# Optimization experiments

Measured on AMD Instinct MI355X. Metric: run time of the kernel, lower is better.

## Reference

```python
import jax, jax.numpy as jnp
import numpy as np

N_KNN = 20
BN_EPS = 1e-5
LRELU_SLOPE = 0.2


def setup_inputs() -> dict:
    key = jax.random.key(0)
    k1, k2, k3 = jax.random.split(key, 3)
    B, C, N = 4, 3, 8192
    x = jax.random.normal(k1, (B, C, N), dtype=jnp.float32)
    # Conv2d(1, 16, 1): weight [16,1,1,1] -> flatten to [16]; bias [16]
    conv_w = jax.random.normal(k2, (16,), dtype=jnp.float32) * (1.0 / np.sqrt(1.0))
    conv_b = jax.random.normal(k3, (16,), dtype=jnp.float32) * 0.01
    gamma = jnp.ones((16,), dtype=jnp.float32)
    beta = jnp.zeros((16,), dtype=jnp.float32)
    return {"x": x, "conv_w": conv_w, "conv_b": conv_b, "gamma": gamma, "beta": beta}


def reference(x, conv_w, conv_b, gamma, beta):
    # x: [B, C, N]
    pts = jnp.transpose(x, (0, 2, 1))  # [B, N, C]
    sq = jnp.sum(pts * pts, axis=-1)  # [B, N]
    # pairwise squared distances, clamped for numerical safety
    d2 = sq[:, :, None] + sq[:, None, :] - 2.0 * jnp.einsum("bnc,bmc->bnm", pts, pts)
    d2 = jnp.maximum(d2, 0.0)
    # safe sqrt: zero gradient at zero distance (matches torch.cdist behavior)
    dist = jnp.where(d2 > 0, jnp.sqrt(jnp.where(d2 > 0, d2, 1.0)), 0.0)  # [B, N, N]
    # k smallest distances = k largest of negated
    neg_topk, _ = jax.lax.top_k(-dist, N_KNN)
    knn = -neg_topk  # [B, N, K], ascending
    # 1x1 conv (1 -> 16 channels): feat[b,c,n,k] = w[c]*knn[b,n,k] + b[c]
    feat = knn[:, None, :, :] * conv_w[None, :, None, None] + conv_b[None, :, None, None]  # [B,16,N,K]
    # BatchNorm2d in training mode: per-channel stats over (B, N, K), biased variance
    mean = jnp.mean(feat, axis=(0, 2, 3), keepdims=True)
    var = jnp.mean((feat - mean) ** 2, axis=(0, 2, 3), keepdims=True)
    xhat = (feat - mean) * jax.lax.rsqrt(var + BN_EPS)
    y = gamma[None, :, None, None] * xhat + beta[None, :, None, None]
    # LeakyReLU(0.2)
    y = jnp.where(y >= 0, y, LRELU_SLOPE * y)
    # max over k neighbors
    return jnp.max(y, axis=-1)  # [B, 16, N]
```

## Files before the change

kernel.cpp:

```cpp
#include <hip/hip_runtime.h>
#include <stdint.h>

#define NPTS  8192
#define NB    4
#define KNN   20
#define NROWS (NB * NPTS)
#define NGROUPS (NROWS / 64)
#define MTOTF 655360.0f
#define WPB   8
#define BLK   (WPB * 64)
#define SLICE (NPTS / WPB)
#define HALF  (NPTS / 2)
#define SLICE2 (HALF / WPB)
#define LSTR  (KNN + 1)
#define CAP   12
#define CAP2  16
#define NGRID (2 * NGROUPS)
#define NEG_INF -3.0e38f

__device__ __forceinline__ float med3f(float a, float b, float c) {
    return __builtin_amdgcn_fmed3f(a, b, c);
}

__device__ __forceinline__ unsigned enc_f(float f) {
    unsigned u = __float_as_uint(f);
    return (u & 0x80000000u) ? ~u : (u | 0x80000000u);
}
__device__ __forceinline__ float dec_f(unsigned u) {
    return __uint_as_float((u & 0x80000000u) ? (u & 0x7fffffffu) : ~u);
}

__device__ __forceinline__ void insert_t(float arr[KNN], float t) {
#pragma unroll
    for (int j = KNN - 1; j > 0; --j) arr[j] = med3f(t, arr[j - 1], arr[j]);
    arr[0] = fmaxf(arr[0], t);
}

__device__ __forceinline__ void flush_buf(float arr[KNN], int& cnt,
    const float* bufw, int lane, unsigned* threshS) {
#pragma unroll
    for (int s = 0; s < CAP; ++s) {
        const float v = bufw[s * 64 + lane];
        insert_t(arr, (s < cnt) ? v : NEG_INF);
    }
    cnt = 0;
    atomicMax(&threshS[lane], enc_f(arr[KNN - 1]));
}

__device__ __forceinline__ void flush_dyn(float arr[KNN], int& cnt,
    const float* bufw, int lane, unsigned* threshS) {
#pragma unroll
    for (int s0 = 0; s0 < CAP2; s0 += 4) {
        if (__any(cnt > s0)) {
#pragma unroll
            for (int s = s0; s < s0 + 4; ++s) {
                const float v = bufw[s * 64 + lane];
                insert_t(arr, (s < cnt) ? v : NEG_INF);
            }
        }
    }
    cnt = 0;
    atomicMax(&threshS[lane], enc_f(arr[KNN - 1]));
}

__device__ __forceinline__ void finalize_row(
    float arr[KNN], float px, float py, float pz, int row, int lane,
    float* __restrict__ kmaxA, float* __restrict__ kminA, float* __restrict__ acc)
{
    const float pn2 = px * px + py * py + pz * pz;
    float sum = 0.f, sum2 = 0.f, dmin = 0.f, dmax = 0.f;
#pragma unroll
    for (int k = 0; k < KNN; ++k) {
        float d2 = fmaxf(fmaf(-2.f, arr[k], pn2), 0.f);
        float d = sqrtf(d2);
        sum += d; sum2 += d2;
        if (k == 0) dmin = d;
        dmax = d;
    }
    kmaxA[row] = dmax;
    kminA[row] = dmin;
#pragma unroll
    for (int o = 32; o; o >>= 1) {
        sum  += __shfl_down(sum,  o, 64);
        sum2 += __shfl_down(sum2, o, 64);
    }
    if (lane == 0) { atomicAdd(acc, sum); atomicAdd(acc + 1, sum2); }
}

__global__ __launch_bounds__(256) void prep_kernel(
    const float* __restrict__ x, float4* __restrict__ tile4,
    float* __restrict__ acc, int* __restrict__ ticket)
{
    const int i = blockIdx.x * 256 + threadIdx.x;
    const int b = i >> 13;
    const int m = i & (NPTS - 1);
    const float* xb = x + b * 3 * NPTS;
    const float qx = xb[m], qy = xb[NPTS + m], qz = xb[2 * NPTS + m];
    tile4[i] = make_float4(qx, qy, qz, -0.5f * (qx * qx + qy * qy + qz * qz));
    if (i < 2) acc[i] = 0.f;
    if (ticket && i < NGROUPS) ticket[i] = 0;
}

__global__ __launch_bounds__(BLK, 8) void knn_fused_kernel(
    const float* __restrict__ x, const float4* __restrict__ tile4,
    float* __restrict__ part, int* __restrict__ ticket,
    float* __restrict__ kmaxA, float* __restrict__ kminA, float* __restrict__ acc)
{
    __shared__ float shmem[WPB * CAP2 * 64];
    __shared__ unsigned threshS[64];

    const int tid  = threadIdx.x;
    const int lane = tid & 63;
    const int wave = __builtin_amdgcn_readfirstlane(tid >> 6);
    const int rb   = blockIdx.x >> 1;
    const int half = blockIdx.x & 1;
    const int rowBase = rb * 64;
    const int row  = rowBase + lane;
    const int b    = rowBase >> 13;
    const int n    = row & (NPTS - 1);
    const float* xb = x + b * 3 * NPTS;
    const float px = xb[n];
    const float py = xb[NPTS + n];
    const float pz = xb[2 * NPTS + n];

    if (tid < 64) threshS[tid] = enc_f(NEG_INF);

    float arr[KNN];
#pragma unroll
    for (int j = 0; j < KNN; ++j) arr[j] = NEG_INF;
    float* bufw = shmem + wave * (CAP2 * 64);
    __syncthreads();

    const float4* __restrict__ tp = tile4 + b * NPTS + half * HALF + wave * SLICE2;

#pragma unroll 8
    for (int i = 0; i < 32; ++i) {
        const float4 q = tp[i];
        insert_t(arr, fmaf(q.x, px, fmaf(q.y, py, fmaf(q.z, pz, q.w))));
    }
    atomicMax(&threshS[lane], enc_f(arr[KNN - 1]));

    int cnt = 0;
    for (int c = 1; c < SLICE2 / 32; ++c) {
        float th = dec_f(*(volatile unsigned*)(threshS + lane));
        const float4* tq = tp + c * 32;
        for (int g = 0; g < 8; ++g) {
#pragma unroll
            for (int u = 0; u < 4; ++u) {
                const float4 q = tq[g * 4 + u];
                const float t = fmaf(q.x, px, fmaf(q.y, py, fmaf(q.z, pz, q.w)));
                bufw[cnt * 64 + lane] = t;
                cnt += (t > th);
            }
            if (__any(cnt > CAP2 - 4)) {
                flush_dyn(arr, cnt, bufw, lane, threshS);
                th = dec_f(*(volatile unsigned*)(threshS + lane));
            }
        }
    }
    if (__any(cnt > 0)) flush_dyn(arr, cnt, bufw, lane, threshS);
    __syncthreads();

    float* ml = shmem;
    if (wave & 1) {
        float* d = ml + (wave >> 1) * (64 * LSTR) + lane * LSTR;
#pragma unroll
        for (int k = 0; k < KNN; ++k) d[k] = arr[k];
    }
    __syncthreads();
    if (!(wave & 1)) {
        const float* s = ml + (wave >> 1) * (64 * LSTR) + lane * LSTR;
#pragma unroll
        for (int k = 0; k < KNN; ++k) insert_t(arr, s[k]);
    }
    __syncthreads();
    if (!(wave & 1) && (wave & 2)) {
        float* d = ml + (wave >> 2) * (64 * LSTR) + lane * LSTR;
#pragma unroll
        for (int k = 0; k < KNN; ++k) d[k] = arr[k];
    }
    __syncthreads();
    if ((wave & 3) == 0) {
        const float* s = ml + (wave >> 2) * (64 * LSTR) + lane * LSTR;
#pragma unroll
        for (int k = 0; k < KNN; ++k) insert_t(arr, s[k]);
    }
    __syncthreads();
    if (wave == 4) {
        float* d = ml + lane * LSTR;
#pragma unroll
        for (int k = 0; k < KNN; ++k) d[k] = arr[k];
    }
    __syncthreads();
    if (wave == 0) {
        const float* s = ml + lane * LSTR;
#pragma unroll
        for (int k = 0; k < KNN; ++k) insert_t(arr, s[k]);

        float* dst = part + (row * 2 + half) * KNN;
#pragma unroll
        for (int k = 0; k < KNN; ++k)
            __hip_atomic_store(&dst[k], arr[k], __ATOMIC_RELAXED,
                               __HIP_MEMORY_SCOPE_AGENT);
        asm volatile("s_waitcnt vmcnt(0)" ::: "memory");

        int old = 0;
        if (lane == 0)
            old = __hip_atomic_fetch_add(&ticket[rb], 1, __ATOMIC_RELAXED,
                                         __HIP_MEMORY_SCOPE_AGENT);
        old = __shfl(old, 0, 64);
        if (old == 1) {
            const float* srcp = part + (row * 2 + (half ^ 1)) * KNN;
#pragma unroll
            for (int k = 0; k < KNN; ++k) {
                const float v = __hip_atomic_load(&srcp[k], __ATOMIC_RELAXED,
                                                  __HIP_MEMORY_SCOPE_AGENT);
                insert_t(arr, v);
            }
            finalize_row(arr, px, py, pz, row, lane, kmaxA, kminA, acc);
        }
    }
}

__global__ __launch_bounds__(256) void out_elem_kernel(
    const float* __restrict__ kmaxA, const float* __restrict__ kminA,
    const float* __restrict__ acc,
    const float* __restrict__ w, const float* __restrict__ gamma,
    const float* __restrict__ beta, float* __restrict__ out)
{
    const int T = blockIdx.x * 256 + threadIdx.x;
    const int n  = T & (NPTS - 1);
    const int bc = T >> 13;
    const int c  = bc & 15;
    const int b  = bc >> 4;
    const float mu  = acc[0] * (1.0f / MTOTF);
    float var = acc[1] * (1.0f / MTOTF) - mu * mu;
    var = fmaxf(var, 0.f);
    const float wc = w[c];
    const float a  = gamma[c] * wc * rsqrtf(wc * wc * var + 1e-5f);
    const float d  = beta[c] - a * mu;
    const float km = (a >= 0.f) ? kmaxA[b * NPTS + n] : kminA[b * NPTS + n];
    float v = a * km + d;
    v = (v >= 0.f) ? v : 0.2f * v;
    out[T] = v;
}


__global__ __launch_bounds__(BLK, 8) void knn_kernel(
    const float* __restrict__ x, const float4* __restrict__ tile4,
    float* __restrict__ kmaxA, float* __restrict__ kminA, float* __restrict__ acc)
{
    __shared__ float shmem[(WPB - 1) * 64 * LSTR];
    __shared__ unsigned threshS[64];

    const int tid  = threadIdx.x;
    const int lane = tid & 63;
    const int wave = __builtin_amdgcn_readfirstlane(tid >> 6);
    const int rowBase = blockIdx.x * 64;
    const int row  = rowBase + lane;
    const int b    = rowBase >> 13;
    const int n    = row & (NPTS - 1);
    const float* xb = x + b * 3 * NPTS;
    const float px = xb[n];
    const float py = xb[NPTS + n];
    const float pz = xb[2 * NPTS + n];

    if (tid < 64) threshS[tid] = enc_f(NEG_INF);

    float arr[KNN];
#pragma unroll
    for (int j = 0; j < KNN; ++j) arr[j] = NEG_INF;
    float* bufw = shmem + wave * (CAP * 64);
    int cnt = 0;
    __syncthreads();

    const float4* __restrict__ tp = tile4 + b * NPTS + wave * SLICE;
    float th = NEG_INF;
    for (int c = 0; c < SLICE / 32; ++c) {
        th = dec_f(*(volatile unsigned*)(threshS + lane));
        const float4* tq = tp + c * 32;
        for (int g = 0; g < 8; ++g) {
#pragma unroll
            for (int u = 0; u < 4; ++u) {
                const float4 q = tq[g * 4 + u];
                const float t = fmaf(q.x, px, fmaf(q.y, py, fmaf(q.z, pz, q.w)));
                if (t > th) { bufw[cnt * 64 + lane] = t; ++cnt; }
            }
            if (__any(cnt > CAP - 4)) {
                flush_buf(arr, cnt, bufw, lane, threshS);
                th = dec_f(*(volatile unsigned*)(threshS + lane));
            }
        }
    }
    if (__any(cnt > 0)) flush_buf(arr, cnt, bufw, lane, threshS);
    __syncthreads();

    if (wave > 0) {
        float* dst = shmem + ((wave - 1) * 64 + lane) * LSTR;
#pragma unroll
        for (int j = 0; j < KNN; ++j) dst[j] = arr[j];
    }
    __syncthreads();

    if (wave == 0) {
        for (int wsrc = 0; wsrc < WPB - 1; ++wsrc) {
            const float* src = shmem + (wsrc * 64 + lane) * LSTR;
#pragma unroll
            for (int k = 0; k < KNN; ++k) insert_t(arr, src[k]);
        }
        finalize_row(arr, px, py, pz, row, lane, kmaxA, kminA, acc);
    }
}

__global__ __launch_bounds__(BLK) void knn_kernel_lds(
    const float* __restrict__ x,
    float* __restrict__ kmaxA, float* __restrict__ kminA, float* __restrict__ acc)
{
    __shared__ float4 tile[2048];
    __shared__ float  lists[(WPB - 1) * 64 * LSTR];

    const int tid  = threadIdx.x;
    const int lane = tid & 63;
    const int wave = tid >> 6;
    const int rowBase = blockIdx.x * 64;
    const int row  = rowBase + lane;
    const int b    = rowBase >> 13;
    const int n    = row & (NPTS - 1);
    const float* xb = x + b * 3 * NPTS;
    const float px = xb[n];
    const float py = xb[NPTS + n];
    const float pz = xb[2 * NPTS + n];

    float arr[KNN];
#pragma unroll
    for (int j = 0; j < KNN; ++j) arr[j] = NEG_INF;

    for (int t0 = 0; t0 < NPTS; t0 += 2048) {
        __syncthreads();
        const int i4 = tid * 4;
        const float4 qx4 = *(const float4*)(xb + t0 + i4);
        const float4 qy4 = *(const float4*)(xb + NPTS + t0 + i4);
        const float4 qz4 = *(const float4*)(xb + 2 * NPTS + t0 + i4);
        tile[i4 + 0] = make_float4(qx4.x, qy4.x, qz4.x, -0.5f * (qx4.x*qx4.x + qy4.x*qy4.x + qz4.x*qz4.x));
        tile[i4 + 1] = make_float4(qx4.y, qy4.y, qz4.y, -0.5f * (qx4.y*qx4.y + qy4.y*qy4.y + qz4.y*qz4.y));
        tile[i4 + 2] = make_float4(qx4.z, qy4.z, qz4.z, -0.5f * (qx4.z*qx4.z + qy4.z*qy4.z + qz4.z*qz4.z));
        tile[i4 + 3] = make_float4(qx4.w, qy4.w, qz4.w, -0.5f * (qx4.w*qx4.w + qy4.w*qy4.w + qz4.w*qz4.w));
        __syncthreads();
        const float4* basep = tile + wave * 256;
#pragma unroll 4
        for (int i = 0; i < 256; ++i) {
            const float4 q = basep[i];
            float t = fmaf(q.x, px, fmaf(q.y, py, fmaf(q.z, pz, q.w)));
            insert_t(arr, t);
        }
    }
    __syncthreads();

    if (wave > 0) {
        float* dst = lists + ((wave - 1) * 64 + lane) * LSTR;
#pragma unroll
        for (int j = 0; j < KNN; ++j) dst[j] = arr[j];
    }
    __syncthreads();

    if (wave == 0) {
        for (int wsrc = 0; wsrc < WPB - 1; ++wsrc) {
            const float* src = lists + (wsrc * 64 + lane) * LSTR;
#pragma unroll
            for (int k = 0; k < KNN; ++k) insert_t(arr, src[k]);
        }
        finalize_row(arr, px, py, pz, row, lane, kmaxA, kminA, acc);
    }
}

__global__ __launch_bounds__(256) void out_kernel(
    const float* __restrict__ kmaxA, const float* __restrict__ kminA,
    const float* __restrict__ acc,
    const float* __restrict__ w, const float* __restrict__ gamma,
    const float* __restrict__ beta, float* __restrict__ out)
{
    const int r = blockIdx.x * 256 + threadIdx.x;
    const int b = r >> 13;
    const int n = r & (NPTS - 1);
    const float mu  = acc[0] * (1.0f / MTOTF);
    float var = acc[1] * (1.0f / MTOTF) - mu * mu;
    var = fmaxf(var, 0.f);
    const float kmax = kmaxA[r];
    const float kmin = kminA[r];
#pragma unroll
    for (int c = 0; c < 16; ++c) {
        const float wc = w[c];
        const float a = gamma[c] * wc * rsqrtf(wc * wc * var + 1e-5f);
        const float d = beta[c] - a * mu;
        float v = a * (a >= 0.f ? kmax : kmin) + d;
        v = (v >= 0.f) ? v : 0.2f * v;
        out[(b * 16 + c) * NPTS + n] = v;
    }
}

extern "C" void kernel_launch(void* const* d_in, const int* in_sizes, int n_in,
                              void* d_out, int out_size, void* d_ws, size_t ws_size,
                              hipStream_t stream)
{
    const float* x     = (const float*)d_in[0];
    const float* w     = (const float*)d_in[1];
    const float* gamma = (const float*)d_in[3];
    const float* beta  = (const float*)d_in[4];
    float* out = (float*)d_out;
    float* ws  = (float*)d_ws;

    float* kmaxA = ws;
    float* kminA = ws + NROWS;
    float* acc   = ws + 2 * NROWS;
    float4* tile4 = (float4*)(ws + 2 * NROWS + 4);
    float* part  = ws + (2 * NROWS + 4) + 4 * NROWS;
    int* ticket  = (int*)(part + (size_t)NROWS * 2 * KNN);
    const size_t need_tile  = (size_t)(2 * NROWS + 4) * 4 + (size_t)NROWS * 16;
    const size_t need_fused = need_tile + (size_t)NROWS * 2 * KNN * 4
                              + (size_t)NGROUPS * 4;

    if (ws_size >= need_fused) {
        prep_kernel<<<NROWS / 256, 256, 0, stream>>>(x, tile4, acc, ticket);
        knn_fused_kernel<<<NGRID, BLK, 0, stream>>>(x, tile4, part, ticket,
                                                    kmaxA, kminA, acc);
        out_elem_kernel<<<(16 * NROWS) / 256, 256, 0, stream>>>(
            kmaxA, kminA, acc, w, gamma, beta, out);
    } else if (ws_size >= need_tile) {
        prep_kernel<<<NROWS / 256, 256, 0, stream>>>(x, tile4, acc, nullptr);
        knn_kernel<<<NROWS / 64, BLK, 0, stream>>>(x, tile4, kmaxA, kminA, acc);
        out_kernel<<<NROWS / 256, 256, 0, stream>>>(kmaxA, kminA, acc, w, gamma, beta, out);
    } else {
        prep_kernel<<<1, 256, 0, stream>>>(x, tile4, acc, nullptr);
        knn_kernel_lds<<<NROWS / 64, BLK, 0, stream>>>(x, kmaxA, kminA, acc);
        out_kernel<<<NROWS / 256, 256, 0, stream>>>(kmaxA, kminA, acc, w, gamma, beta, out);
    }
}
```

Measured before the change: 190.6 us.

## Process two query rows per lane with 16-wave blocks in fused KNN kernel

Each lane now keeps two top-K lists, one for each of two query rows, so every candidate float4 loaded from the tile is reused for two distance evaluations. Blocks grow to 16 waves over 128 rows, each wave scanning a smaller slice of half the points. Candidate buffers shrink to 9 slots per row, and the cross-wave merge becomes a tree over column-major LDS lists. The aim is to halve tile loads per distance and raise ILP, at the cost of doubled register pressure (two 20-entry arrays per lane), more frequent flushes and a longer sync-heavy merge.

```diff
diff --git a/kernel.cpp b/kernel.cpp
--- a/kernel.cpp
+++ b/kernel.cpp
@@ -10,13 +10,17 @@
 #define WPB   8
 #define BLK   (WPB * 64)
 #define SLICE (NPTS / WPB)
-#define HALF  (NPTS / 2)
-#define SLICE2 (HALF / WPB)
 #define LSTR  (KNN + 1)
 #define CAP   12
-#define CAP2  16
-#define NGRID (2 * NGROUPS)
 #define NEG_INF -3.0e38f
+
+#define WPB2  16
+#define BLK2  (WPB2 * 64)
+#define HALF2 (NPTS / 2)
+#define WSL   (HALF2 / WPB2)
+#define CAPH  9
+#define NGROUPS2 (NROWS / 128)
+#define NGRID2   (2 * NGROUPS2)
 
 __device__ __forceinline__ float med3f(float a, float b, float c) {
     return __builtin_amdgcn_fmed3f(a, b, c);
@@ -47,20 +51,20 @@
     atomicMax(&threshS[lane], enc_f(arr[KNN - 1]));
 }
 
-__device__ __forceinline__ void flush_dyn(float arr[KNN], int& cnt,
-    const float* bufw, int lane, unsigned* threshS) {
-#pragma unroll
-    for (int s0 = 0; s0 < CAP2; s0 += 4) {
+__device__ __forceinline__ void flush_h(float arr[KNN], int& cnt,
+    const float* bufw, unsigned* thp, int lane) {
+#pragma unroll
+    for (int s0 = 0; s0 < CAPH; s0 += 3) {
         if (__any(cnt > s0)) {
 #pragma unroll
-            for (int s = s0; s < s0 + 4; ++s) {
+            for (int s = s0; s < s0 + 3; ++s) {
                 const float v = bufw[s * 64 + lane];
                 insert_t(arr, (s < cnt) ? v : NEG_INF);
             }
         }
     }
     cnt = 0;
-    atomicMax(&threshS[lane], enc_f(arr[KNN - 1]));
+    atomicMax(thp + lane, enc_f(arr[KNN - 1]));
 }
 
 __device__ __forceinline__ void finalize_row(
@@ -85,6 +89,21 @@
         sum2 += __shfl_down(sum2, o, 64);
     }
     if (lane == 0) { atomicAdd(acc, sum); atomicAdd(acc + 1, sum2); }
+}
+
+__device__ __forceinline__ void list_write(float* ml, int slot, int lane,
+    const float a0[KNN], const float a1[KNN]) {
+#pragma unroll
+    for (int k = 0; k < KNN; ++k) ml[((slot * 2 + 0) * KNN + k) * 64 + lane] = a0[k];
+#pragma unroll
+    for (int k = 0; k < KNN; ++k) ml[((slot * 2 + 1) * KNN + k) * 64 + lane] = a1[k];
+}
+__device__ __forceinline__ void list_merge(const float* ml, int slot, int lane,
+    float a0[KNN], float a1[KNN]) {
+#pragma unroll
+    for (int k = 0; k < KNN; ++k) insert_t(a0, ml[((slot * 2 + 0) * KNN + k) * 64 + lane]);
+#pragma unroll
+    for (int k = 0; k < KNN; ++k) insert_t(a1, ml[((slot * 2 + 1) * KNN + k) * 64 + lane]);
 }
 
 __global__ __launch_bounds__(256) void prep_kernel(
@@ -101,106 +120,109 @@
     if (ticket && i < NGROUPS) ticket[i] = 0;
 }
 
-__global__ __launch_bounds__(BLK, 8) void knn_fused_kernel(
+__global__ __launch_bounds__(BLK2, 8) void knn2_kernel(
     const float* __restrict__ x, const float4* __restrict__ tile4,
     float* __restrict__ part, int* __restrict__ ticket,
     float* __restrict__ kmaxA, float* __restrict__ kminA, float* __restrict__ acc)
 {
-    __shared__ float shmem[WPB * CAP2 * 64];
-    __shared__ unsigned threshS[64];
+    __shared__ float shmem[WPB2 * 2 * CAPH * 64];
+    __shared__ unsigned threshS[128];
 
     const int tid  = threadIdx.x;
     const int lane = tid & 63;
     const int wave = __builtin_amdgcn_readfirstlane(tid >> 6);
     const int rb   = blockIdx.x >> 1;
     const int half = blockIdx.x & 1;
-    const int rowBase = rb * 64;
-    const int row  = rowBase + lane;
+    const int rowBase = rb * 128;
+    const int row0 = rowBase + lane;
+    const int row1 = row0 + 64;
     const int b    = rowBase >> 13;
-    const int n    = row & (NPTS - 1);
+    const int n0   = row0 & (NPTS - 1);
+    const int n1   = n0 + 64;
     const float* xb = x + b * 3 * NPTS;
-    const float px = xb[n];
-    const float py = xb[NPTS + n];
-    const float pz = xb[2 * NPTS + n];
-
-    if (tid < 64) threshS[tid] = enc_f(NEG_INF);
-
-    float arr[KNN];
-#pragma unroll
-    for (int j = 0; j < KNN; ++j) arr[j] = NEG_INF;
-    float* bufw = shmem + wave * (CAP2 * 64);
-    __syncthreads();
-
-    const float4* __restrict__ tp = tile4 + b * NPTS + half * HALF + wave * SLICE2;
-
-#pragma unroll 8
+    const float px0 = xb[n0], py0 = xb[NPTS + n0], pz0 = xb[2 * NPTS + n0];
+    const float px1 = xb[n1], py1 = xb[NPTS + n1], pz1 = xb[2 * NPTS + n1];
+
+    if (tid < 128) threshS[tid] = enc_f(NEG_INF);
+
+    float a0[KNN], a1[KNN];
+#pragma unroll
+    for (int j = 0; j < KNN; ++j) { a0[j] = NEG_INF; a1[j] = NEG_INF; }
+    float* buf0 = shmem + wave * (2 * CAPH * 64);
+    float* buf1 = buf0 + CAPH * 64;
+    __syncthreads();
+
+    const float4* __restrict__ tp = tile4 + b * NPTS + half * HALF2 + wave * WSL;
+
+#pragma unroll 4
     for (int i = 0; i < 32; ++i) {
         const float4 q = tp[i];
-        insert_t(arr, fmaf(q.x, px, fmaf(q.y, py, fmaf(q.z, pz, q.w))));
-    }
-    atomicMax(&threshS[lane], enc_f(arr[KNN - 1]));
-
-    int cnt = 0;
-    for (int c = 1; c < SLICE2 / 32; ++c) {
-        float th = dec_f(*(volatile unsigned*)(threshS + lane));
+        insert_t(a0, fmaf(q.x, px0, fmaf(q.y, py0, fmaf(q.z, pz0, q.w))));
+        insert_t(a1, fmaf(q.x, px1, fmaf(q.y, py1, fmaf(q.z, pz1, q.w))));
+    }
+    atomicMax(&threshS[lane],      enc_f(a0[KNN - 1]));
+    atomicMax(&threshS[64 + lane], enc_f(a1[KNN - 1]));
+
+    int c0 = 0, c1 = 0;
+    for (int c = 1; c < WSL / 32; ++c) {
+        float th0 = dec_f(*(volatile unsigned*)(threshS + lane));
+        float th1 = dec_f(*(volatile unsigned*)(threshS + 64 + lane));
         const float4* tq = tp + c * 32;
         for (int g = 0; g < 8; ++g) {
 #pragma unroll
             for (int u = 0; u < 4; ++u) {
                 const float4 q = tq[g * 4 + u];
-                const float t = fmaf(q.x, px, fmaf(q.y, py, fmaf(q.z, pz, q.w)));
-                bufw[cnt * 64 + lane] = t;
-                cnt += (t > th);
-            }
-            if (__any(cnt > CAP2 - 4)) {
-                flush_dyn(arr, cnt, bufw, lane, threshS);
-                th = dec_f(*(volatile unsigned*)(threshS + lane));
-            }
-        }
-    }
-    if (__any(cnt > 0)) flush_dyn(arr, cnt, bufw, lane, threshS);
+                const float t0 = fmaf(q.x, px0, fmaf(q.y, py0, fmaf(q.z, pz0, q.w)));
+                const float t1 = fmaf(q.x, px1, fmaf(q.y, py1, fmaf(q.z, pz1, q.w)));
+                buf0[c0 * 64 + lane] = t0;  c0 += (t0 > th0);
+                buf1[c1 * 64 + lane] = t1;  c1 += (t1 > th1);
+            }
+            if (__any(c0 > CAPH - 4)) {
+                flush_h(a0, c0, buf0, threshS, lane);
+                th0 = dec_f(*(volatile unsigned*)(threshS + lane));
+            }
+            if (__any(c1 > CAPH - 4)) {
+                flush_h(a1, c1, buf1, threshS + 64, lane);
+                th1 = dec_f(*(volatile unsigned*)(threshS + 64 + lane));
+            }
+        }
+    }
+    if (__any(c0 > 0)) flush_h(a0, c0, buf0, threshS, lane);
+    if (__any(c1 > 0)) flush_h(a1, c1, buf1, threshS + 64, lane);
     __syncthreads();
 
     float* ml = shmem;
-    if (wave & 1) {
-        float* d = ml + (wave >> 1) * (64 * LSTR) + lane * LSTR;
-#pragma unroll
-        for (int k = 0; k < KNN; ++k) d[k] = arr[k];
-    }
-    __syncthreads();
-    if (!(wave & 1)) {
-        const float* s = ml + (wave >> 1) * (64 * LSTR) + lane * LSTR;
-#pragma unroll
-        for (int k = 0; k < KNN; ++k) insert_t(arr, s[k]);
-    }
-    __syncthreads();
-    if (!(wave & 1) && (wave & 2)) {
-        float* d = ml + (wave >> 2) * (64 * LSTR) + lane * LSTR;
-#pragma unroll
-        for (int k = 0; k < KNN; ++k) d[k] = arr[k];
-    }
-    __syncthreads();
-    if ((wave & 3) == 0) {
-        const float* s = ml + (wave >> 2) * (64 * LSTR) + lane * LSTR;
-#pragma unroll
-        for (int k = 0; k < KNN; ++k) insert_t(arr, s[k]);
-    }
-    __syncthreads();
-    if (wave == 4) {
-        float* d = ml + lane * LSTR;
-#pragma unroll
-        for (int k = 0; k < KNN; ++k) d[k] = arr[k];
-    }
-    __syncthreads();
+    if (wave >= 8 && wave < 12) list_write(ml, wave - 8, lane, a0, a1);
+    __syncthreads();
+    if (wave < 4) list_merge(ml, wave, lane, a0, a1);
+    __syncthreads();
+    if (wave >= 12) list_write(ml, wave - 12, lane, a0, a1);
+    __syncthreads();
+    if (wave >= 4 && wave < 8) list_merge(ml, wave - 4, lane, a0, a1);
+    __syncthreads();
+    if (wave >= 4 && wave < 8) list_write(ml, wave - 4, lane, a0, a1);
+    __syncthreads();
+    if (wave < 4) list_merge(ml, wave, lane, a0, a1);
+    __syncthreads();
+    if (wave == 2 || wave == 3) list_write(ml, wave - 2, lane, a0, a1);
+    __syncthreads();
+    if (wave < 2) list_merge(ml, wave, lane, a0, a1);
+    __syncthreads();
+    if (wave == 1) list_write(ml, 0, lane, a0, a1);
+    __syncthreads();
+
     if (wave == 0) {
-        const float* s = ml + lane * LSTR;
-#pragma unroll
-        for (int k = 0; k < KNN; ++k) insert_t(arr, s[k]);
-
-        float* dst = part + (row * 2 + half) * KNN;
+        list_merge(ml, 0, lane, a0, a1);
+
+        float* d0 = part + (row0 * 2 + half) * KNN;
+        float* d1 = part + (row1 * 2 + half) * KNN;
 #pragma unroll
         for (int k = 0; k < KNN; ++k)
-            __hip_atomic_store(&dst[k], arr[k], __ATOMIC_RELAXED,
+            __hip_atomic_store(&d0[k], a0[k], __ATOMIC_RELAXED,
+                               __HIP_MEMORY_SCOPE_AGENT);
+#pragma unroll
+        for (int k = 0; k < KNN; ++k)
+            __hip_atomic_store(&d1[k], a1[k], __ATOMIC_RELAXED,
                                __HIP_MEMORY_SCOPE_AGENT);
         asm volatile("s_waitcnt vmcnt(0)" ::: "memory");
 
@@ -210,14 +232,18 @@
                                          __HIP_MEMORY_SCOPE_AGENT);
         old = __shfl(old, 0, 64);
         if (old == 1) {
-            const float* srcp = part + (row * 2 + (half ^ 1)) * KNN;
-#pragma unroll
-            for (int k = 0; k < KNN; ++k) {
-                const float v = __hip_atomic_load(&srcp[k], __ATOMIC_RELAXED,
-                                                  __HIP_MEMORY_SCOPE_AGENT);
-                insert_t(arr, v);
-            }
-            finalize_row(arr, px, py, pz, row, lane, kmaxA, kminA, acc);
+            const float* s0p = part + (row0 * 2 + (half ^ 1)) * KNN;
+            const float* s1p = part + (row1 * 2 + (half ^ 1)) * KNN;
+#pragma unroll
+            for (int k = 0; k < KNN; ++k)
+                insert_t(a0, __hip_atomic_load(&s0p[k], __ATOMIC_RELAXED,
+                                               __HIP_MEMORY_SCOPE_AGENT));
+#pragma unroll
+            for (int k = 0; k < KNN; ++k)
+                insert_t(a1, __hip_atomic_load(&s1p[k], __ATOMIC_RELAXED,
+                                               __HIP_MEMORY_SCOPE_AGENT));
+            finalize_row(a0, px0, py0, pz0, row0, lane, kmaxA, kminA, acc);
+            finalize_row(a1, px1, py1, pz1, row1, lane, kmaxA, kminA, acc);
         }
     }
 }
@@ -421,8 +447,8 @@
 
     if (ws_size >= need_fused) {
         prep_kernel<<<NROWS / 256, 256, 0, stream>>>(x, tile4, acc, ticket);
-        knn_fused_kernel<<<NGRID, BLK, 0, stream>>>(x, tile4, part, ticket,
-                                                    kmaxA, kminA, acc);
+        knn2_kernel<<<NGRID2, BLK2, 0, stream>>>(x, tile4, part, ticket,
+                                                 kmaxA, kminA, acc);
         out_elem_kernel<<<(16 * NROWS) / 256, 256, 0, stream>>>(
             kmaxA, kminA, acc, w, gamma, beta, out);
     } else if (ws_size >= need_tile) {
```

After: 221.7 us. +16.3%, slower.

## Bin-sort points by x and prune KNN scan with sorted-order early exit

Applied to the files above, without the earlier changes.

Adds a per-batch counting-sort kernel that buckets points by x coordinate into 256 bins and writes sorted float4 tiles plus a permutation. The KNN kernel then scans outward from each 64-row group in sorted order, one block per direction, and stops once the bin boundary of the next chunk lies beyond the current k-th distance bound. The goal is to skip most of the brute-force O(N^2) distance work. The cost is a serial single-block-per-batch sort, extra block-wide syncs per phase, and pruning efficiency that depends on how the points are distributed.

```diff
diff --git a/kernel.cpp b/kernel.cpp
--- a/kernel.cpp
+++ b/kernel.cpp
@@ -10,12 +10,14 @@
 #define WPB   8
 #define BLK   (WPB * 64)
 #define SLICE (NPTS / WPB)
-#define HALF  (NPTS / 2)
-#define SLICE2 (HALF / WPB)
 #define LSTR  (KNN + 1)
 #define CAP   12
 #define CAP2  16
 #define NGRID (2 * NGROUPS)
+#define MAXPH (NPTS / 256)
+#define NBIN  256
+#define BINW  0.03125f
+#define XLO   -4.0f
 #define NEG_INF -3.0e38f
 
 __device__ __forceinline__ float med3f(float a, float b, float c) {
@@ -87,41 +89,75 @@
     if (lane == 0) { atomicAdd(acc, sum); atomicAdd(acc + 1, sum2); }
 }
 
-__global__ __launch_bounds__(256) void prep_kernel(
-    const float* __restrict__ x, float4* __restrict__ tile4,
-    float* __restrict__ acc, int* __restrict__ ticket)
-{
-    const int i = blockIdx.x * 256 + threadIdx.x;
-    const int b = i >> 13;
-    const int m = i & (NPTS - 1);
+__global__ __launch_bounds__(1024) void sort_kernel(
+    const float* __restrict__ x, float4* __restrict__ sorted4,
+    int* __restrict__ perm, float* __restrict__ acc, int* __restrict__ ticket)
+{
+    __shared__ int hist[NBIN];
+    __shared__ int cursor[NBIN];
+    const int b = blockIdx.x;
+    const int tid = threadIdx.x;
+    if (tid < NBIN) hist[tid] = 0;
+    if (b == 0) {
+        if (tid < 2) acc[tid] = 0.f;
+        if (tid < NGROUPS) ticket[tid] = 0;
+    }
+    __syncthreads();
     const float* xb = x + b * 3 * NPTS;
-    const float qx = xb[m], qy = xb[NPTS + m], qz = xb[2 * NPTS + m];
-    tile4[i] = make_float4(qx, qy, qz, -0.5f * (qx * qx + qy * qy + qz * qz));
-    if (i < 2) acc[i] = 0.f;
-    if (ticket && i < NGROUPS) ticket[i] = 0;
-}
-
-__global__ __launch_bounds__(BLK, 8) void knn_fused_kernel(
-    const float* __restrict__ x, const float4* __restrict__ tile4,
+    int bins[8];
+#pragma unroll
+    for (int k = 0; k < 8; ++k) {
+        const int i = tid + k * 1024;
+        int bin = (int)floorf((xb[i] - XLO) * 32.0f);
+        bin = min(max(bin, 0), NBIN - 1);
+        bins[k] = bin;
+        atomicAdd(&hist[bin], 1);
+    }
+    __syncthreads();
+    int cnt0 = (tid < NBIN) ? hist[tid] : 0;
+    for (int off = 1; off < NBIN; off <<= 1) {
+        int v = (tid < NBIN && tid >= off) ? hist[tid - off] : 0;
+        __syncthreads();
+        if (tid < NBIN) hist[tid] += v;
+        __syncthreads();
+    }
+    if (tid < NBIN) cursor[tid] = hist[tid] - cnt0;
+    __syncthreads();
+#pragma unroll
+    for (int k = 0; k < 8; ++k) {
+        const int i = tid + k * 1024;
+        const float qx = xb[i];
+        const float qy = xb[NPTS + i];
+        const float qz = xb[2 * NPTS + i];
+        const int pos = atomicAdd(&cursor[bins[k]], 1);
+        sorted4[b * NPTS + pos] =
+            make_float4(qx, qy, qz, -0.5f * (qx * qx + qy * qy + qz * qz));
+        perm[b * NPTS + pos] = b * NPTS + i;
+    }
+}
+
+__global__ __launch_bounds__(BLK, 8) void knn_sorted_kernel(
+    const float4* __restrict__ sorted4, const int* __restrict__ perm,
     float* __restrict__ part, int* __restrict__ ticket,
     float* __restrict__ kmaxA, float* __restrict__ kminA, float* __restrict__ acc)
 {
     __shared__ float shmem[WPB * CAP2 * 64];
     __shared__ unsigned threshS[64];
+    __shared__ int doneS;
 
     const int tid  = threadIdx.x;
     const int lane = tid & 63;
     const int wave = __builtin_amdgcn_readfirstlane(tid >> 6);
     const int rb   = blockIdx.x >> 1;
-    const int half = blockIdx.x & 1;
-    const int rowBase = rb * 64;
-    const int row  = rowBase + lane;
-    const int b    = rowBase >> 13;
-    const int n    = row & (NPTS - 1);
-    const float* xb = x + b * 3 * NPTS;
-    const float px = xb[n];
-    const float py = xb[NPTS + n];
-    const float pz = xb[2 * NPTS + n];
+    const int side = blockIdx.x & 1;
+    const int base0 = rb * 64;
+    const int b    = base0 >> 13;
+    const int batchBegin = b * NPTS;
+    const int batchEnd   = batchBegin + NPTS;
+
+    const float4 P = sorted4[base0 + lane];
+    const float px = P.x, py = P.y, pz = P.z;
+    const float pn2 = -2.f * P.w;
 
     if (tid < 64) threshS[tid] = enc_f(NEG_INF);
 
@@ -129,43 +165,74 @@
 #pragma unroll
     for (int j = 0; j < KNN; ++j) arr[j] = NEG_INF;
     float* bufw = shmem + wave * (CAP2 * 64);
-    __syncthreads();
-
-    const float4* __restrict__ tp = tile4 + b * NPTS + half * HALF + wave * SLICE2;
-
-#pragma unroll 8
-    for (int i = 0; i < 32; ++i) {
-        const float4 q = tp[i];
-        insert_t(arr, fmaf(q.x, px, fmaf(q.y, py, fmaf(q.z, pz, q.w))));
-    }
-    atomicMax(&threshS[lane], enc_f(arr[KNN - 1]));
-
     int cnt = 0;
-    for (int c = 1; c < SLICE2 / 32; ++c) {
+    __syncthreads();
+
+    for (int p = 0; p < MAXPH; ++p) {
+        const int ci = p * WPB + wave;
+        const int cs = (side == 0) ? base0 + ci * 32 : base0 - (ci + 1) * 32;
+        const bool valid = (side == 0) ? (cs < batchEnd) : (cs >= batchBegin);
         float th = dec_f(*(volatile unsigned*)(threshS + lane));
-        const float4* tq = tp + c * 32;
-        for (int g = 0; g < 8; ++g) {
-#pragma unroll
-            for (int u = 0; u < 4; ++u) {
-                const float4 q = tq[g * 4 + u];
-                const float t = fmaf(q.x, px, fmaf(q.y, py, fmaf(q.z, pz, q.w)));
-                bufw[cnt * 64 + lane] = t;
-                cnt += (t > th);
+        if (valid) {
+            const float4* tq = sorted4 + cs;
+            for (int g = 0; g < 8; ++g) {
+#pragma unroll
+                for (int u = 0; u < 4; ++u) {
+                    const float4 q = tq[g * 4 + u];
+                    const float t = fmaf(q.x, px, fmaf(q.y, py, fmaf(q.z, pz, q.w)));
+                    bufw[cnt * 64 + lane] = t;
+                    cnt += (t > th);
+                }
+                if (__any(cnt > CAP2 - 4)) {
+                    flush_dyn(arr, cnt, bufw, lane, threshS);
+                    th = dec_f(*(volatile unsigned*)(threshS + lane));
+                }
             }
-            if (__any(cnt > CAP2 - 4)) {
-                flush_dyn(arr, cnt, bufw, lane, threshS);
-                th = dec_f(*(volatile unsigned*)(threshS + lane));
+        }
+        if (tid == 0) doneS = 1;
+        __syncthreads();
+
+        const float th2 = dec_f(*(volatile unsigned*)(threshS + lane));
+        const float d2  = fmaxf(fmaf(-2.f, th2, pn2), 0.f);
+        const float d   = sqrtf(d2);
+        bool myDone;
+        if (side == 0) {
+            float need = px + d;
+#pragma unroll
+            for (int o = 32; o; o >>= 1) need = fmaxf(need, __shfl_xor(need, o, 64));
+            const int f = base0 + (p + 1) * 256;
+            if (f >= batchEnd) myDone = true;
+            else {
+                const float xf = sorted4[f].x;
+                int bf = (int)floorf((xf - XLO) * 32.0f);
+                bf = min(max(bf, 0), NBIN - 1);
+                myDone = (bf > 0) && ((float)bf * BINW + XLO >= need);
             }
-        }
+        } else {
+            float need = px - d;
+#pragma unroll
+            for (int o = 32; o; o >>= 1) need = fminf(need, __shfl_xor(need, o, 64));
+            const int f = base0 - (p + 1) * 256;
+            if (f <= batchBegin) myDone = true;
+            else {
+                const float xf = sorted4[f - 1].x;
+                int bf = (int)floorf((xf - XLO) * 32.0f);
+                bf = min(max(bf, 0), NBIN - 1);
+                myDone = (bf < NBIN - 1) && ((float)(bf + 1) * BINW + XLO <= need);
+            }
+        }
+        if (lane == 0 && !myDone) doneS = 0;
+        __syncthreads();
+        if (doneS) break;
     }
     if (__any(cnt > 0)) flush_dyn(arr, cnt, bufw, lane, threshS);
     __syncthreads();
 
     float* ml = shmem;
     if (wave & 1) {
-        float* d = ml + (wave >> 1) * (64 * LSTR) + lane * LSTR;
-#pragma unroll
-        for (int k = 0; k < KNN; ++k) d[k] = arr[k];
+        float* dl = ml + (wave >> 1) * (64 * LSTR) + lane * LSTR;
+#pragma unroll
+        for (int k = 0; k < KNN; ++k) dl[k] = arr[k];
     }
     __syncthreads();
     if (!(wave & 1)) {
@@ -175,9 +242,9 @@
     }
     __syncthreads();
     if (!(wave & 1) && (wave & 2)) {
-        float* d = ml + (wave >> 2) * (64 * LSTR) + lane * LSTR;
-#pragma unroll
-        for (int k = 0; k < KNN; ++k) d[k] = arr[k];
+        float* dl = ml + (wave >> 2) * (64 * LSTR) + lane * LSTR;
+#pragma unroll
+        for (int k = 0; k < KNN; ++k) dl[k] = arr[k];
     }
     __syncthreads();
     if ((wave & 3) == 0) {
@@ -187,9 +254,9 @@
     }
     __syncthreads();
     if (wave == 4) {
-        float* d = ml + lane * LSTR;
-#pragma unroll
-        for (int k = 0; k < KNN; ++k) d[k] = arr[k];
+        float* dl = ml + lane * LSTR;
+#pragma unroll
+        for (int k = 0; k < KNN; ++k) dl[k] = arr[k];
     }
     __syncthreads();
     if (wave == 0) {
@@ -197,7 +264,8 @@
 #pragma unroll
         for (int k = 0; k < KNN; ++k) insert_t(arr, s[k]);
 
-        float* dst = part + (row * 2 + half) * KNN;
+        const int srow = base0 + lane;
+        float* dst = part + (srow * 2 + side) * KNN;
 #pragma unroll
         for (int k = 0; k < KNN; ++k)
             __hip_atomic_store(&dst[k], arr[k], __ATOMIC_RELAXED,
@@ -210,14 +278,13 @@
                                          __HIP_MEMORY_SCOPE_AGENT);
         old = __shfl(old, 0, 64);
         if (old == 1) {
-            const float* srcp = part + (row * 2 + (half ^ 1)) * KNN;
-#pragma unroll
-            for (int k = 0; k < KNN; ++k) {
-                const float v = __hip_atomic_load(&srcp[k], __ATOMIC_RELAXED,
-                                                  __HIP_MEMORY_SCOPE_AGENT);
-                insert_t(arr, v);
-            }
-            finalize_row(arr, px, py, pz, row, lane, kmaxA, kminA, acc);
+            const float* sp = part + (srow * 2 + (side ^ 1)) * KNN;
+#pragma unroll
+            for (int k = 0; k < KNN; ++k)
+                insert_t(arr, __hip_atomic_load(&sp[k], __ATOMIC_RELAXED,
+                                                __HIP_MEMORY_SCOPE_AGENT));
+            const int orow = perm[srow];
+            finalize_row(arr, px, py, pz, orow, lane, kmaxA, kminA, acc);
         }
     }
 }
@@ -245,6 +312,18 @@
     out[T] = v;
 }
 
+
+__global__ __launch_bounds__(256) void prep_kernel(
+    const float* __restrict__ x, float4* __restrict__ tile4, float* __restrict__ acc)
+{
+    const int i = blockIdx.x * 256 + threadIdx.x;
+    const int b = i >> 13;
+    const int m = i & (NPTS - 1);
+    const float* xb = x + b * 3 * NPTS;
+    const float qx = xb[m], qy = xb[NPTS + m], qz = xb[2 * NPTS + m];
+    tile4[i] = make_float4(qx, qy, qz, -0.5f * (qx * qx + qy * qy + qz * qz));
+    if (i < 2) acc[i] = 0.f;
+}
 
 __global__ __launch_bounds__(BLK, 8) void knn_kernel(
     const float* __restrict__ x, const float4* __restrict__ tile4,
@@ -412,25 +491,28 @@
     float* kmaxA = ws;
     float* kminA = ws + NROWS;
     float* acc   = ws + 2 * NROWS;
-    float4* tile4 = (float4*)(ws + 2 * NROWS + 4);
-    float* part  = ws + (2 * NROWS + 4) + 4 * NROWS;
-    int* ticket  = (int*)(part + (size_t)NROWS * 2 * KNN);
-    const size_t need_tile  = (size_t)(2 * NROWS + 4) * 4 + (size_t)NROWS * 16;
-    const size_t need_fused = need_tile + (size_t)NROWS * 2 * KNN * 4
-                              + (size_t)NGROUPS * 4;
-
-    if (ws_size >= need_fused) {
-        prep_kernel<<<NROWS / 256, 256, 0, stream>>>(x, tile4, acc, ticket);
-        knn_fused_kernel<<<NGRID, BLK, 0, stream>>>(x, tile4, part, ticket,
-                                                    kmaxA, kminA, acc);
+    float4* sorted4 = (float4*)(ws + 2 * NROWS + 4);
+    int*   perm  = (int*)(ws + (2 * NROWS + 4) + 4 * NROWS);
+    float* part  = (float*)(perm + NROWS);
+    int*   ticket = (int*)(part + (size_t)NROWS * 2 * KNN);
+
+    const size_t need_tile   = (size_t)(2 * NROWS + 4) * 4 + (size_t)NROWS * 16;
+    const size_t need_sorted = need_tile + (size_t)NROWS * 4
+                               + (size_t)NROWS * 2 * KNN * 4 + (size_t)NGROUPS * 4;
+
+    if (ws_size >= need_sorted) {
+        sort_kernel<<<NB, 1024, 0, stream>>>(x, sorted4, perm, acc, ticket);
+        knn_sorted_kernel<<<NGRID, BLK, 0, stream>>>(sorted4, perm, part, ticket,
+                                                     kmaxA, kminA, acc);
         out_elem_kernel<<<(16 * NROWS) / 256, 256, 0, stream>>>(
             kmaxA, kminA, acc, w, gamma, beta, out);
     } else if (ws_size >= need_tile) {
-        prep_kernel<<<NROWS / 256, 256, 0, stream>>>(x, tile4, acc, nullptr);
+        float4* tile4 = sorted4;
+        prep_kernel<<<NROWS / 256, 256, 0, stream>>>(x, tile4, acc);
         knn_kernel<<<NROWS / 64, BLK, 0, stream>>>(x, tile4, kmaxA, kminA, acc);
         out_kernel<<<NROWS / 256, 256, 0, stream>>>(kmaxA, kminA, acc, w, gamma, beta, out);
     } else {
-        prep_kernel<<<1, 256, 0, stream>>>(x, tile4, acc, nullptr);
+        prep_kernel<<<1, 256, 0, stream>>>(x, sorted4, acc);
         knn_kernel_lds<<<NROWS / 64, BLK, 0, stream>>>(x, kmaxA, kminA, acc);
         out_kernel<<<NROWS / 256, 256, 0, stream>>>(kmaxA, kminA, acc, w, gamma, beta, out);
     }
```

Result: slower. 245.6 us (+28.8%).
